# Optimization experiments

Measured on AMD Instinct MI355X. Metric: run time of the kernel, lower is better.

The kernel has to match this reference:

```python
import jax, jax.numpy as jnp
import numpy as np

# ---- constants mirroring init_kwargs ----
S = 128          # sheet_units
KA = 25          # aff_cf_units
C = 2            # aff_cf_channels
KL = 25          # lat_cf_units
EXC = 9          # exc_units
DA = 1           # aff_cf_dilation
DL = 1           # lat_cf_dilation
HOMEO_TARGET = 0.04
STRENGTH = 1.0

# ---- radial helper masks (get_circle / get_radial_cos) ----
def _dist(n):
    g = jnp.arange(n, dtype=jnp.float32) - (n - 1) / 2.0
    return jnp.sqrt(g[:, None] ** 2 + g[None, :] ** 2)

def _circle(n, r):
    return (_dist(n) < r).astype(jnp.float32)

def _rcos(n, wl):
    return jnp.cos(_dist(n) * jnp.pi / wl)

# afferent envelope: [C*KA*KA], channel-major like torch repeat+view
_ae = _rcos(KA, KA) ** 2 * _circle(KA, KA / 2)
_ae = _ae / _ae.max()
AFF_ENV = jnp.tile(_ae.reshape(1, KA * KA), (C, 1)).reshape(C * KA * KA)

# lateral (LRI) envelope: [KL*KL]
_inh = _rcos(KL, EXC / DL) ** 2 * _circle(KL, EXC / (2 * DL))
_le = _rcos(KL, KL) ** 2 * (1.0 - _inh) * _circle(KL, KL / 2)
LRI_ENV = (_le / _le.max()).reshape(KL * KL)

def _unfold(x, k, dil):
    """x: [C,H,W] -> patches [L, C*k*k], torch F.unfold ordering (C slowest)."""
    Cc, H, W = x.shape
    out = H - dil * (k - 1)
    idx = jnp.arange(out)[:, None] + dil * jnp.arange(k)[None, :]  # [out,k]
    p = x[:, idx, :]          # [C,out,k,W]
    p = p[:, :, :, idx]       # [C,out,k,out,k]
    p = p.transpose(1, 3, 0, 2, 4)  # [out_i,out_j,C,ki,kj]
    return p.reshape(out * out, Cc * k * k)

def setup_inputs() -> dict:
    key = jax.random.key(0)
    k1, k2 = jax.random.split(key)
    in_size = S + DA * (KA - 1)  # 152
    x = jax.random.uniform(k1, (1, C, in_size, in_size), dtype=jnp.float32)
    rfs = jax.random.uniform(k2, (S * S, C * KA * KA, 1), dtype=jnp.float32)
    rfs = rfs / rfs.sum(1, keepdims=True)
    lat_weights = jnp.ones((S * S, KL * KL, 1), jnp.float32) / (KL * KL)
    adathresh = jnp.zeros((1, 1, S, S), jnp.float32)
    return {"x": x, "rfs": rfs, "lat_weights": lat_weights, "adathresh": adathresh}

def _forward(x, rfs, lat_weights, adathresh):
    relu = jax.nn.relu
    rfs = relu(rfs)                 # no_grad positive clamp of params
    lw = relu(lat_weights)
    # afferent: unfold + envelope + per-pixel dot (bmm with [L,F,1])
    tiles = _unfold(x[0], KA, DA) * AFF_ENV[None, :]          # [L, C*KA*KA]
    raw_aff = jnp.einsum('lf,lf->l', tiles, rfs[:, :, 0]).reshape(S, S)
    aff = jax.lax.stop_gradient(raw_aff) - adathresh[0, 0]
    lat = relu(aff)
    # lateral inhibition: pad so unfold yields S*S positions
    p = DL * (KL - 1) // 2
    lt = _unfold(jnp.pad(lat, p)[None], KL, DL) * LRI_ENV[None, :]  # [L, KL*KL]
    lat_neg = jnp.einsum('lf,lf->l', lt, jax.lax.stop_gradient(lw)[:, :, 0]).reshape(S, S)
    lat = lat - lat_neg
    lat = jnp.tanh(relu(lat * STRENGTH + aff))
    # hebbian lateral correlations term (learning_flag path)
    lt2 = _unfold(jnp.pad(lat, p, constant_values=HOMEO_TARGET)[None], KL, DL) * LRI_ENV[None, :]
    weighted = lt2 * lat.reshape(S * S, 1)
    lat_correlations = jnp.einsum('lf,lf->', weighted, lw[:, :, 0])
    return (raw_aff.reshape(1, 1, S, S), lat.reshape(1, 1, S, S),
            lat_correlations, tiles[:, None, :])

def reference(x, rfs, lat_weights, adathresh):
    return _forward(x, rfs, lat_weights, adathresh)
```

## Files before the change

### kernel.cpp

```cpp
#include <hip/hip_runtime.h>
#include <math.h>

#define S 128
#define KA 25
#define PATCH 625
#define FEAT 1250
#define PI_F 3.14159265358979323846f
#define PADW 152
#define PADA (PADW * PADW)

#define WS_LRI 0
#define WS_AE 640
#define WS_LAT0P 1280
#define WS_LATFP 24384
#define WS_PART 47488
#define NPART 1024

__device__ __forceinline__ int div25(int r) { return (r * 10486) >> 18; }

__device__ __forceinline__ void gld16(const float* g, float* l) {
    __builtin_amdgcn_global_load_lds(
        (const __attribute__((address_space(1))) void*)g,
        (__attribute__((address_space(3))) void*)l, 16, 0, 0);
}
#define VMCNT(N) asm volatile("s_waitcnt vmcnt(" #N ")" ::: "memory"); \
                 __builtin_amdgcn_sched_barrier(0)

__global__ __launch_bounds__(256) void k_init(float* __restrict__ ws) {
    const int tid = threadIdx.x;
    if (blockIdx.x == 0) {
        __shared__ float s_tmp[640];
        __shared__ float s_red[4];
        float m = 0.0f;
        for (int r = tid; r < PATCH; r += 256) {
            int qi = div25(r);
            float di = (float)qi - 12.0f;
            float dj = (float)(r - 25 * qi) - 12.0f;
            float d = sqrtf(di * di + dj * dj);
            float ae = 0.0f, le = 0.0f;
            if (d < 12.5f) {
                float c1 = cosf(d * (PI_F / 25.0f));
                ae = c1 * c1;
                float inh = 0.0f;
                if (d < 4.5f) {
                    float c2 = cosf(d * (PI_F / 9.0f));
                    inh = c2 * c2;
                }
                le = c1 * c1 * (1.0f - inh);
            }
            ws[WS_AE + r] = ae;
            s_tmp[r] = le;
            m = fmaxf(m, le);
        }
        for (int o = 32; o; o >>= 1) m = fmaxf(m, __shfl_down(m, o));
        if (!(tid & 63)) s_red[tid >> 6] = m;
        __syncthreads();
        float inv = 1.0f / fmaxf(fmaxf(s_red[0], s_red[1]),
                                 fmaxf(s_red[2], s_red[3]));
        for (int r = tid; r < PATCH; r += 256) ws[WS_LRI + r] = s_tmp[r] * inv;
    }
    const int gid = blockIdx.x * 256 + tid;
    const int gsz = gridDim.x * 256;
    for (int i = gid; i < 2 * PADA; i += gsz) {
        if (i < PADA) ws[WS_LAT0P + i] = 0.0f;
        else          ws[WS_LATFP + i - PADA] = 0.04f;
    }
}

__global__ __launch_bounds__(256) void k_afftiles(const float* __restrict__ x,
                                                  const float* __restrict__ rfs,
                                                  const float* __restrict__ ada,
                                                  float* __restrict__ raw_aff,
                                                  float* __restrict__ tiles,
                                                  float* __restrict__ ws) {
    __shared__ float s_ae[640];
    __shared__ float s_x[2][25][40];
    __shared__ float s_st[4][2][1280];
    const int tid = threadIdx.x, lane = tid & 63, wv = tid >> 6;
    const int blk = blockIdx.x;
    const int li = blk >> 3;
    const int lj0 = (blk & 7) << 4;

    for (int i = tid; i < 625; i += 256) s_ae[i] = ws[WS_AE + i];
    for (int i = tid; i < 2000; i += 256) {
        int c = i >= 1000;
        int rm = i - (c ? 1000 : 0);
        int ki = rm / 40;
        int col = rm - ki * 40;
        s_x[c][ki][col] = x[c * PADA + (li + ki) * PADW + lj0 + col];
    }
    __syncthreads();

    const int tc0 = wv << 2;
    const int l0 = li * 128 + lj0 + tc0;

    float acc_ht[4], ad[4];
#define HT(n) { \
        const int l = l0 + (n); const long B = (long)l * FEAT; \
        const int peel = (l & 1) ? 2 : 0; \
        float a = 0.0f; \
        if (lane < 2) { \
            int f = peel ? lane : (1248 + lane); \
            int c = f >= 625; int r = f - (c ? 625 : 0); \
            int ki = div25(r); int kj = r - 25 * ki; \
            float t = s_x[c][ki][kj + tc0 + (n)] * s_ae[r]; \
            tiles[B + f] = t; \
            a = t * fmaxf(rfs[B + f], 0.0f); \
        } \
        if (!lane) ad[n] = ada[l]; \
        acc_ht[n] = a; }
    HT(0) HT(1) HT(2) HT(3)
#undef HT

    auto stage = [&](int n, float* buf) {
        const int l = l0 + n;
        const long B = (long)l * FEAT;
        const int peel = (l & 1) ? 2 : 0;
        const float* gp = rfs + B + peel + 4 * lane;
        gld16(gp,        buf);
        gld16(gp + 256,  buf + 256);
        gld16(gp + 512,  buf + 512);
        gld16(gp + 768,  buf + 768);
        if (lane < 56) gld16(gp + 1024, buf + 1024);
    };
    auto consume = [&](int n, const float* buf, float accin, float adv) {
        const int l = l0 + n;
        const long B = (long)l * FEAT;
        const int peel = (l & 1) ? 2 : 0;
        const int tc = tc0 + n;
        float acc = accin;
#pragma unroll
        for (int j = 0; j < 20; ++j) {
            int fh = j * 64 + lane;
            if (j < 19 || lane < 32) {
                float rv = buf[fh];
                int f = peel + fh;
                int c = f >= 625;
                int r = f - (c ? 625 : 0);
                int ki = div25(r);
                int kj = r - 25 * ki;
                float t = s_x[c][ki][kj + tc] * s_ae[r];
                tiles[B + f] = t;
                acc += t * fmaxf(rv, 0.0f);
            }
        }
        for (int o = 32; o; o >>= 1) acc += __shfl_down(acc, o);
        if (!lane) {
            raw_aff[l] = acc;
            ws[WS_LAT0P + (li + 12) * PADW + lj0 + tc + 12] =
                fmaxf(acc - adv, 0.0f);
        }
    };

    float* buf0 = &s_st[wv][0][0];
    float* buf1 = &s_st[wv][1][0];
    __builtin_amdgcn_sched_barrier(0);
    stage(0, buf0);
    stage(1, buf1);
    VMCNT(5);
    consume(0, buf0, acc_ht[0], ad[0]);
    stage(2, buf0);
    VMCNT(27);
    consume(1, buf1, acc_ht[1], ad[1]);
    stage(3, buf1);
    VMCNT(27);
    consume(2, buf0, acc_ht[2], ad[2]);
    VMCNT(22);
    consume(3, buf1, acc_ht[3], ad[3]);
}

__global__ __launch_bounds__(256) void k_lat(const float* __restrict__ raw_aff,
                                             const float* __restrict__ ada,
                                             const float* __restrict__ lw,
                                             float* __restrict__ latf,
                                             float* __restrict__ ws) {
    __shared__ float s_le[640];
    __shared__ float s_g[25][40];
    __shared__ float s_st[4][2][640];
    const int tid = threadIdx.x, lane = tid & 63, wv = tid >> 6;
    const int blk = blockIdx.x;
    const int li = blk >> 3;
    const int lj0 = (blk & 7) << 4;

    for (int i = tid; i < 625; i += 256) s_le[i] = ws[WS_LRI + i];
    for (int i = tid; i < 1000; i += 256) {
        int ki = i / 40;
        int col = i - ki * 40;
        s_g[ki][col] = ws[WS_LAT0P + (li + ki) * PADW + lj0 + col];
    }
    __syncthreads();

    const int tc0 = wv << 2;
    const int l0 = li * 128 + lj0 + tc0;

    float acc_ht[4], ra[4], ad[4];
#define HT(n) { \
        const int l = l0 + (n); const long B = (long)l * PATCH; \
        const int peel = (4 - (l & 3)) & 3; \
        const int fmax4 = (PATCH - peel) & ~3; \
        const int tcnt = (PATCH - peel) & 3; \
        float a = 0.0f; \
        if (lane < peel) { \
            int f = lane; int ki = div25(f); int kj = f - 25 * ki; \
            a += s_g[ki][kj + tc0 + (n)] * s_le[f] * fmaxf(lw[B + f], 0.0f); \
        } \
        if (lane < tcnt) { \
            int f = peel + fmax4 + lane; int ki = div25(f); int kj = f - 25 * ki; \
            a += s_g[ki][kj + tc0 + (n)] * s_le[f] * fmaxf(lw[B + f], 0.0f); \
        } \
        if (!lane) { ra[n] = raw_aff[l]; ad[n] = ada[l]; } \
        acc_ht[n] = a; }
    HT(0) HT(1) HT(2) HT(3)
#undef HT

    auto stage = [&](int n, float* buf) {
        const int l = l0 + n;
        const long B = (long)l * PATCH;
        const int peel = (4 - (l & 3)) & 3;
        const int rem = ((PATCH - peel) >> 2) - 128;
        const float* gp = lw + B + peel + 4 * lane;
        gld16(gp,       buf);
        gld16(gp + 256, buf + 256);
        if (lane < rem) gld16(gp + 512, buf + 512);
    };
    auto consume = [&](int n, const float* buf, float accin, float rav,
                       float adv) {
        const int l = l0 + n;
        const int peel = (4 - (l & 3)) & 3;
        const int fmax4 = (PATCH - peel) & ~3;
        const int tc = tc0 + n;
        float acc = accin;
#pragma unroll
        for (int j = 0; j < 10; ++j) {
            int fh = j * 64 + lane;
            if (j < 9 || fh < fmax4) {
                float wval = buf[fh];
                int f = peel + fh;
                int ki = div25(f);
                int kj = f - 25 * ki;
                acc += s_g[ki][kj + tc] * s_le[f] * fmaxf(wval, 0.0f);
            }
        }
        for (int o = 32; o; o >>= 1) acc += __shfl_down(acc, o);
        if (!lane) {
            float aff_l = rav - adv;
            float lat0_l = fmaxf(aff_l, 0.0f);
            float v = (lat0_l - acc)  + aff_l;
            float lv = tanhf(fmaxf(v, 0.0f));
            latf[l] = lv;
            ws[WS_LATFP + (li + 12) * PADW + lj0 + tc + 12] = lv;
        }
    };

    float* buf0 = &s_st[wv][0][0];
    float* buf1 = &s_st[wv][1][0];
    __builtin_amdgcn_sched_barrier(0);
    stage(0, buf0);
    stage(1, buf1);
    VMCNT(3);
    consume(0, buf0, acc_ht[0], ra[0], ad[0]);
    stage(2, buf0);
    VMCNT(5);
    consume(1, buf1, acc_ht[1], ra[1], ad[1]);
    stage(3, buf1);
    VMCNT(5);
    consume(2, buf0, acc_ht[2], ra[2], ad[2]);
    VMCNT(2);
    consume(3, buf1, acc_ht[3], ra[3], ad[3]);
}

__global__ __launch_bounds__(256) void k_corr(const float* __restrict__ latf,
                                              const float* __restrict__ lw,
                                              float* __restrict__ ws) {
    __shared__ float s_le[640];
    __shared__ float s_g[25][40];
    __shared__ float s_st[4][2][640];
    __shared__ float s_red[4];
    const int tid = threadIdx.x, lane = tid & 63, wv = tid >> 6;
    const int blk = blockIdx.x;
    const int li = blk >> 3;
    const int lj0 = (blk & 7) << 4;

    for (int i = tid; i < 625; i += 256) s_le[i] = ws[WS_LRI + i];
    for (int i = tid; i < 1000; i += 256) {
        int ki = i / 40;
        int col = i - ki * 40;
        s_g[ki][col] = ws[WS_LATFP + (li + ki) * PADW + lj0 + col];
    }
    __syncthreads();

    const int tc0 = wv << 2;
    const int l0 = li * 128 + lj0 + tc0;

    float acc_ht[4], lf[4];
#define HT(n) { \
        const int l = l0 + (n); const long B = (long)l * PATCH; \
        const int peel = (4 - (l & 3)) & 3; \
        const int fmax4 = (PATCH - peel) & ~3; \
        const int tcnt = (PATCH - peel) & 3; \
        float a = 0.0f; \
        if (lane < peel) { \
            int f = lane; int ki = div25(f); int kj = f - 25 * ki; \
            a += s_g[ki][kj + tc0 + (n)] * s_le[f] * fmaxf(lw[B + f], 0.0f); \
        } \
        if (lane < tcnt) { \
            int f = peel + fmax4 + lane; int ki = div25(f); int kj = f - 25 * ki; \
            a += s_g[ki][kj + tc0 + (n)] * s_le[f] * fmaxf(lw[B + f], 0.0f); \
        } \
        if (!lane) lf[n] = latf[l]; \
        acc_ht[n] = a; }
    HT(0) HT(1) HT(2) HT(3)
#undef HT

    auto stage = [&](int n, float* buf) {
        const int l = l0 + n;
        const long B = (long)l * PATCH;
        const int peel = (4 - (l & 3)) & 3;
        const int rem = ((PATCH - peel) >> 2) - 128;
        const float* gp = lw + B + peel + 4 * lane;
        gld16(gp,       buf);
        gld16(gp + 256, buf + 256);
        if (lane < rem) gld16(gp + 512, buf + 512);
    };
    float wsum = 0.0f;
    auto consume = [&](int n, const float* buf, float accin, float lfv) {
        const int l = l0 + n;
        const int peel = (4 - (l & 3)) & 3;
        const int fmax4 = (PATCH - peel) & ~3;
        const int tc = tc0 + n;
        float acc = accin;
#pragma unroll
        for (int j = 0; j < 10; ++j) {
            int fh = j * 64 + lane;
            if (j < 9 || fh < fmax4) {
                float wval = buf[fh];
                int f = peel + fh;
                int ki = div25(f);
                int kj = f - 25 * ki;
                acc += s_g[ki][kj + tc] * s_le[f] * fmaxf(wval, 0.0f);
            }
        }
        for (int o = 32; o; o >>= 1) acc += __shfl_down(acc, o);
        if (!lane) wsum += acc * lfv;
    };

    float* buf0 = &s_st[wv][0][0];
    float* buf1 = &s_st[wv][1][0];
    __builtin_amdgcn_sched_barrier(0);
    stage(0, buf0);
    stage(1, buf1);
    VMCNT(3);
    consume(0, buf0, acc_ht[0], lf[0]);
    stage(2, buf0);
    VMCNT(3);
    consume(1, buf1, acc_ht[1], lf[1]);
    stage(3, buf1);
    VMCNT(3);
    consume(2, buf0, acc_ht[2], lf[2]);
    VMCNT(0);
    consume(3, buf1, acc_ht[3], lf[3]);

    if (!lane) s_red[wv] = wsum;
    __syncthreads();
    if (!tid)
        ws[WS_PART + blk] = s_red[0] + s_red[1] + s_red[2] + s_red[3];
}

__global__ __launch_bounds__(256) void k_reduce(const float* __restrict__ ws,
                                                float* __restrict__ corr) {
    __shared__ float s_red[4];
    const int tid = threadIdx.x;
    const int lane = tid & 63, wv = tid >> 6;
    float acc = 0.0f;
    for (int i = tid; i < NPART; i += 256) acc += ws[WS_PART + i];
    for (int o = 32; o; o >>= 1) acc += __shfl_down(acc, o);
    if (!lane) s_red[wv] = acc;
    __syncthreads();
    if (!tid) corr[0] = s_red[0] + s_red[1] + s_red[2] + s_red[3];
}

extern "C" void kernel_launch(void* const* d_in, const int* in_sizes, int n_in,
                              void* d_out, int out_size, void* d_ws, size_t ws_size,
                              hipStream_t stream) {
    const float* x   = (const float*)d_in[0];
    const float* rfs = (const float*)d_in[1];
    const float* lw  = (const float*)d_in[2];
    const float* ada = (const float*)d_in[3];

    float* out      = (float*)d_out;
    float* raw_aff  = out;
    float* latf     = out + S * S;
    float* corr     = out + 2 * S * S;
    float* tiles    = out + 2 * S * S + 1;
    float* ws       = (float*)d_ws;

    k_init<<<16, 256, 0, stream>>>(ws);
    k_afftiles<<<1024, 256, 0, stream>>>(x, rfs, ada, raw_aff, tiles, ws);
    k_lat<<<1024, 256, 0, stream>>>(raw_aff, ada, lw, latf, ws);
    k_corr<<<1024, 256, 0, stream>>>(latf, lw, ws);
    k_reduce<<<1, 256, 0, stream>>>(ws, corr);
}
```

Measured before the change: 225.3 us.

## Split tile writes across kernels and simplify afferent kernel to direct loads

The afferent kernel now processes one pixel per wavefront over a 4096-block grid. It loads rfs directly as float4 into registers instead of staging through LDS with async loads, and reads x straight from global memory. It writes only channel-0 tiles. The channel-1 tile writes move into epilogues of the lateral and correlation kernels, split by even and odd rows, so that the large tiles store traffic overlaps with those bandwidth-lighter kernels. The afferent envelope is also stored in a permuted slot layout to reduce LDS bank conflicts, at the cost of extra global x reads and added work in the later kernels.

After: 223.6 us. Within noise of the previous version (-0.8%).

```diff
diff --git a/kernel.cpp b/kernel.cpp
--- a/kernel.cpp
+++ b/kernel.cpp
@@ -17,6 +17,7 @@
 #define NPART 1024
 
 __device__ __forceinline__ int div25(int r) { return (r * 10486) >> 18; }
+__device__ __forceinline__ int eslot(int r) { return (r & 3) * 160 + (r >> 2); }
 
 __device__ __forceinline__ void gld16(const float* g, float* l) {
     __builtin_amdgcn_global_load_lds(
@@ -48,7 +49,7 @@
                 }
                 le = c1 * c1 * (1.0f - inh);
             }
-            ws[WS_AE + r] = ae;
+            ws[WS_AE + eslot(r)] = ae;
             s_tmp[r] = le;
             m = fmaxf(m, le);
         }
@@ -67,112 +68,103 @@
     }
 }
 
-__global__ __launch_bounds__(256) void k_afftiles(const float* __restrict__ x,
-                                                  const float* __restrict__ rfs,
-                                                  const float* __restrict__ ada,
-                                                  float* __restrict__ raw_aff,
-                                                  float* __restrict__ tiles,
-                                                  float* __restrict__ ws) {
+__global__ __launch_bounds__(256) void k_aff(const float* __restrict__ x,
+                                             const float* __restrict__ rfs,
+                                             const float* __restrict__ ada,
+                                             float* __restrict__ raw_aff,
+                                             float* __restrict__ tiles,
+                                             float* __restrict__ ws) {
     __shared__ float s_ae[640];
-    __shared__ float s_x[2][25][40];
-    __shared__ float s_st[4][2][1280];
-    const int tid = threadIdx.x, lane = tid & 63, wv = tid >> 6;
-    const int blk = blockIdx.x;
-    const int li = blk >> 3;
-    const int lj0 = (blk & 7) << 4;
-
-    for (int i = tid; i < 625; i += 256) s_ae[i] = ws[WS_AE + i];
-    for (int i = tid; i < 2000; i += 256) {
-        int c = i >= 1000;
-        int rm = i - (c ? 1000 : 0);
-        int ki = rm / 40;
-        int col = rm - ki * 40;
-        s_x[c][ki][col] = x[c * PADA + (li + ki) * PADW + lj0 + col];
-    }
-    __syncthreads();
-
-    const int tc0 = wv << 2;
-    const int l0 = li * 128 + lj0 + tc0;
-
-    float acc_ht[4], ad[4];
-#define HT(n) { \
-        const int l = l0 + (n); const long B = (long)l * FEAT; \
-        const int peel = (l & 1) ? 2 : 0; \
-        float a = 0.0f; \
-        if (lane < 2) { \
-            int f = peel ? lane : (1248 + lane); \
-            int c = f >= 625; int r = f - (c ? 625 : 0); \
-            int ki = div25(r); int kj = r - 25 * ki; \
-            float t = s_x[c][ki][kj + tc0 + (n)] * s_ae[r]; \
-            tiles[B + f] = t; \
-            a = t * fmaxf(rfs[B + f], 0.0f); \
-        } \
-        if (!lane) ad[n] = ada[l]; \
-        acc_ht[n] = a; }
-    HT(0) HT(1) HT(2) HT(3)
-#undef HT
-
-    auto stage = [&](int n, float* buf) {
-        const int l = l0 + n;
-        const long B = (long)l * FEAT;
-        const int peel = (l & 1) ? 2 : 0;
-        const float* gp = rfs + B + peel + 4 * lane;
-        gld16(gp,        buf);
-        gld16(gp + 256,  buf + 256);
-        gld16(gp + 512,  buf + 512);
-        gld16(gp + 768,  buf + 768);
-        if (lane < 56) gld16(gp + 1024, buf + 1024);
+    const int tid = threadIdx.x;
+    for (int i = tid; i < 640; i += 256) s_ae[i] = ws[WS_AE + i];
+    __syncthreads();
+
+    const int lane = tid & 63;
+    const int l = blockIdx.x * 4 + (tid >> 6);
+    const int li = l >> 7, lj = l & 127;
+    const int wb = li * PADW + lj;
+    const long B = (long)l * FEAT;
+    const int peel = (l & 1) ? 2 : 0;
+
+    float acc = 0.0f;
+    if (lane < peel) {
+        int f = lane;
+        float t = x[wb + f] * s_ae[eslot(f)];
+        tiles[B + f] = t;
+        acc += t * fmaxf(rfs[B + f], 0.0f);
+    }
+
+    const float* __restrict__ rb = rfs + B + peel;
+    const float4 rv0 = *reinterpret_cast<const float4*>(rb + 4 * lane);
+    const float4 rv1 = *reinterpret_cast<const float4*>(rb + 4 * (lane + 64));
+    const float4 rv2 = *reinterpret_cast<const float4*>(rb + 4 * (lane + 128));
+    const float4 rv3 = *reinterpret_cast<const float4*>(rb + 4 * (lane + 192));
+    float4 rv4 = {0.0f, 0.0f, 0.0f, 0.0f};
+    if (lane < 56) rv4 = *reinterpret_cast<const float4*>(rb + 4 * (lane + 256));
+
+    auto consume = [&](const float4& rv, int k) {
+        const int f0 = peel + 4 * k;
+#pragma unroll
+        for (int j = 0; j < 4; ++j) {
+            int f = f0 + j;
+            int c = (f >= PATCH) ? 1 : 0;
+            int r = f - c * PATCH;
+            float t = x[c * PADA + wb + r + 127 * div25(r)] * s_ae[eslot(r)];
+            if (f < PATCH) tiles[B + f] = t;
+            acc += t * fmaxf((&rv.x)[j], 0.0f);
+        }
     };
-    auto consume = [&](int n, const float* buf, float accin, float adv) {
-        const int l = l0 + n;
-        const long B = (long)l * FEAT;
-        const int peel = (l & 1) ? 2 : 0;
+    consume(rv0, lane);
+    consume(rv1, lane + 64);
+    consume(rv2, lane + 128);
+    consume(rv3, lane + 192);
+    if (lane < 56) consume(rv4, lane + 256);
+
+    if (lane < 2 - peel) {
+        int f = 1248 + lane;
+        int r = f - PATCH;
+        acc += x[PADA + wb + r + 127 * div25(r)] * s_ae[eslot(r)]
+               * fmaxf(rfs[B + f], 0.0f);
+    }
+
+    for (int o = 32; o; o >>= 1) acc += __shfl_down(acc, o);
+    if (!lane) {
+        raw_aff[l] = acc;
+        ws[WS_LAT0P + (li + 12) * PADW + (lj + 12)] = fmaxf(acc - ada[l], 0.0f);
+    }
+}
+
+__device__ __forceinline__ void tiles_c1_epilogue(
+        const float* __restrict__ x, float* __restrict__ tiles,
+        const float* __restrict__ ws, float* e_ae, float* e_x1,
+        int li, int lj0, int tc0, int lane, int tid) {
+    for (int i = tid; i < 640; i += 256) e_ae[i] = ws[WS_AE + i];
+    for (int i = tid; i < 1000; i += 256) {
+        int ki = i / 40, col = i - ki * 40;
+        e_x1[i] = x[PADA + (li + ki) * PADW + lj0 + col];
+    }
+    __syncthreads();
+#pragma unroll
+    for (int n = 0; n < 4; ++n) {
         const int tc = tc0 + n;
-        float acc = accin;
+        const long B = (long)(li * 128 + lj0 + tc) * FEAT + PATCH;
 #pragma unroll
-        for (int j = 0; j < 20; ++j) {
-            int fh = j * 64 + lane;
-            if (j < 19 || lane < 32) {
-                float rv = buf[fh];
-                int f = peel + fh;
-                int c = f >= 625;
-                int r = f - (c ? 625 : 0);
-                int ki = div25(r);
-                int kj = r - 25 * ki;
-                float t = s_x[c][ki][kj + tc] * s_ae[r];
-                tiles[B + f] = t;
-                acc += t * fmaxf(rv, 0.0f);
+        for (int j = 0; j < 10; ++j) {
+            int r = j * 64 + lane;
+            if (j < 9 || lane < 49) {
+                int ki = div25(r), kj = r - 25 * ki;
+                tiles[B + r] = e_x1[ki * 40 + kj + tc] * e_ae[eslot(r)];
             }
         }
-        for (int o = 32; o; o >>= 1) acc += __shfl_down(acc, o);
-        if (!lane) {
-            raw_aff[l] = acc;
-            ws[WS_LAT0P + (li + 12) * PADW + lj0 + tc + 12] =
-                fmaxf(acc - adv, 0.0f);
-        }
-    };
-
-    float* buf0 = &s_st[wv][0][0];
-    float* buf1 = &s_st[wv][1][0];
-    __builtin_amdgcn_sched_barrier(0);
-    stage(0, buf0);
-    stage(1, buf1);
-    VMCNT(5);
-    consume(0, buf0, acc_ht[0], ad[0]);
-    stage(2, buf0);
-    VMCNT(27);
-    consume(1, buf1, acc_ht[1], ad[1]);
-    stage(3, buf1);
-    VMCNT(27);
-    consume(2, buf0, acc_ht[2], ad[2]);
-    VMCNT(22);
-    consume(3, buf1, acc_ht[3], ad[3]);
+    }
 }
 
 __global__ __launch_bounds__(256) void k_lat(const float* __restrict__ raw_aff,
                                              const float* __restrict__ ada,
                                              const float* __restrict__ lw,
+                                             const float* __restrict__ x,
                                              float* __restrict__ latf,
+                                             float* __restrict__ tiles,
                                              float* __restrict__ ws) {
     __shared__ float s_le[640];
     __shared__ float s_g[25][40];
@@ -267,10 +259,18 @@
     consume(2, buf0, acc_ht[2], ra[2], ad[2]);
     VMCNT(2);
     consume(3, buf1, acc_ht[3], ra[3], ad[3]);
+
+    if ((li & 1) == 0) {
+        __syncthreads();
+        tiles_c1_epilogue(x, tiles, ws, &s_st[0][0][0], &s_st[1][0][0],
+                          li, lj0, tc0, lane, tid);
+    }
 }
 
 __global__ __launch_bounds__(256) void k_corr(const float* __restrict__ latf,
                                               const float* __restrict__ lw,
+                                              const float* __restrict__ x,
+                                              float* __restrict__ tiles,
                                               float* __restrict__ ws) {
     __shared__ float s_le[640];
     __shared__ float s_g[25][40];
@@ -364,6 +364,12 @@
     __syncthreads();
     if (!tid)
         ws[WS_PART + blk] = s_red[0] + s_red[1] + s_red[2] + s_red[3];
+
+    if ((li & 1) == 1) {
+        __syncthreads();
+        tiles_c1_epilogue(x, tiles, ws, &s_st[0][0][0], &s_st[1][0][0],
+                          li, lj0, tc0, lane, tid);
+    }
 }
 
 __global__ __launch_bounds__(256) void k_reduce(const float* __restrict__ ws,
@@ -395,8 +401,8 @@
     float* ws       = (float*)d_ws;
 
     k_init<<<16, 256, 0, stream>>>(ws);
-    k_afftiles<<<1024, 256, 0, stream>>>(x, rfs, ada, raw_aff, tiles, ws);
-    k_lat<<<1024, 256, 0, stream>>>(raw_aff, ada, lw, latf, ws);
-    k_corr<<<1024, 256, 0, stream>>>(latf, lw, ws);
+    k_aff<<<4096, 256, 0, stream>>>(x, rfs, ada, raw_aff, tiles, ws);
+    k_lat<<<1024, 256, 0, stream>>>(raw_aff, ada, lw, x, latf, tiles, ws);
+    k_corr<<<1024, 256, 0, stream>>>(latf, lw, x, tiles, ws);
     k_reduce<<<1, 256, 0, stream>>>(ws, corr);
 }
```
